# Kernel optimization log

Measured on AMD Instinct MI355X. Metric: run time of the kernel, lower is better.

Reference implementation:

```python
import jax, jax.numpy as jnp
import numpy as np

N = 100000   # nodes
E = 1600000  # edges
D = 128      # input_dim
H = 128      # hidden_dim
O = 128      # output_dim
G = 64       # graphs in batch
BN_EPS = 1e-5


def setup_inputs() -> dict:
    key = jax.random.key(0)
    ks = jax.random.split(key, 32)
    x = jax.random.normal(ks[0], (N, D), jnp.float32)
    edge_index = jax.random.randint(ks[1], (2, E), 0, N, dtype=jnp.int64)
    batch = jnp.sort(jax.random.randint(ks[2], (N,), 0, G, dtype=jnp.int64))

    def lin_w(k, fan_in, fan_out):
        return (jax.random.normal(k, (fan_in, fan_out), jnp.float32) / np.sqrt(fan_in)).astype(jnp.float32)

    def lin_b(k, fan_out):
        return (0.01 * jax.random.normal(k, (fan_out,), jnp.float32)).astype(jnp.float32)

    def bn(k, dim):
        k1, k2, k3, k4 = jax.random.split(k, 4)
        gamma = 1.0 + 0.1 * jax.random.normal(k1, (dim,), jnp.float32)
        beta = 0.1 * jax.random.normal(k2, (dim,), jnp.float32)
        mean = 0.1 * jax.random.normal(k3, (dim,), jnp.float32)
        var = 0.5 + jax.random.uniform(k4, (dim,), jnp.float32)
        return gamma, beta, mean, var

    inp = {
        "x": x, "edge_index": edge_index, "batch": batch,
        "w11": lin_w(ks[3], D, H), "b11": lin_b(ks[4], H),
        "w12": lin_w(ks[5], H, H), "b12": lin_b(ks[6], H),
        "w21": lin_w(ks[7], H, H), "b21": lin_b(ks[8], H),
        "w22": lin_w(ks[9], H, H), "b22": lin_b(ks[10], H),
        "w31": lin_w(ks[11], H, H), "b31": lin_b(ks[12], H),
        "w32": lin_w(ks[13], H, O), "b32": lin_b(ks[14], O),
    }
    g1, be1, m1, v1 = bn(ks[15], H)
    g2, be2, m2, v2 = bn(ks[16], H)
    g3, be3, m3, v3 = bn(ks[17], O)
    inp.update({"bn1_g": g1, "bn1_b": be1, "bn1_m": m1, "bn1_v": v1,
                "bn2_g": g2, "bn2_b": be2, "bn2_m": m2, "bn2_v": v2,
                "bn3_g": g3, "bn3_b": be3, "bn3_m": m3, "bn3_v": v3})
    return inp


def _gin_conv(x, src, dst, wa, ba, wb, bb):
    # sum-aggregate neighbor features: out[i] = x[i] + sum_{(j->i) in E} x[j]  (eps=0)
    agg = jax.ops.segment_sum(x[src], dst, num_segments=N)
    h = x + agg
    # 2-layer MLP: Linear -> ReLU -> Linear
    return jax.nn.relu(h @ wa + ba) @ wb + bb


def _bn_eval(x, g, b, m, v):
    return (x - m) * (g * jax.lax.rsqrt(v + BN_EPS)) + b


def reference(x, edge_index, batch,
              w11, b11, w12, b12, w21, b21, w22, b22, w31, b31, w32, b32,
              bn1_g, bn1_b, bn1_m, bn1_v,
              bn2_g, bn2_b, bn2_m, bn2_v,
              bn3_g, bn3_b, bn3_m, bn3_v):
    src, dst = edge_index[0], edge_index[1]
    h = _gin_conv(x, src, dst, w11, b11, w12, b12)
    h = jax.nn.relu(_bn_eval(h, bn1_g, bn1_b, bn1_m, bn1_v))  # dropout: eval-mode identity
    h = _gin_conv(h, src, dst, w21, b21, w22, b22)
    h = jax.nn.relu(_bn_eval(h, bn2_g, bn2_b, bn2_m, bn2_v))
    h = _gin_conv(h, src, dst, w31, b31, w32, b32)
    h = jax.nn.relu(_bn_eval(h, bn3_g, bn3_b, bn3_m, bn3_v))
    # global mean pool over each graph
    sums = jax.ops.segment_sum(h, batch, num_segments=G)
    counts = jax.ops.segment_sum(jnp.ones((N,), h.dtype), batch, num_segments=G)
    return sums / jnp.maximum(counts, 1.0)[:, None]
```

## Files before the change

### kernel.cpp

```cpp
#include <hip/hip_runtime.h>
#include <hip/hip_bf16.h>
#include <cstdint>

static constexpr int D = 128;
static constexpr int SPANB = 9;
static constexpr int CHUNK = 4096;

typedef __bf16 v8bf __attribute__((ext_vector_type(8)));
typedef float  v4f  __attribute__((ext_vector_type(4)));

__device__ inline float bflo(unsigned u) { return __uint_as_float(u << 16); }
__device__ inline float bfhi(unsigned u) { return __uint_as_float(u & 0xffff0000u); }
__device__ inline unsigned short bfbits(float f) {
    __hip_bfloat16 h = __float2bfloat16(f);
    return *reinterpret_cast<unsigned short*>(&h);
}
__device__ inline unsigned packbf(float a, float b) {
    return (unsigned)bfbits(a) | ((unsigned)bfbits(b) << 16);
}

__global__ __launch_bounds__(256) void prep_kernel(
    const float* __restrict__ w11, const float* __restrict__ w12,
    const float* __restrict__ w21, const float* __restrict__ w22,
    const float* __restrict__ w31, const float* __restrict__ w32,
    __hip_bfloat16* __restrict__ Wp,
    const float* bn1g, const float* bn1b, const float* bn1m, const float* bn1v, const float* lb1,
    const float* bn2g, const float* bn2b, const float* bn2m, const float* bn2v, const float* lb2,
    const float* bn3g, const float* bn3b, const float* bn3m, const float* bn3v, const float* lb3,
    float* sc1, float* sh1, float* sc2, float* sh2, float* sc3, float* sh3,
    const float* __restrict__ x, __hip_bfloat16* __restrict__ xb, long long n8,
    const int* __restrict__ dst, int* __restrict__ blockhist, int nE, int nblk) {
    int b = blockIdx.x, t = threadIdx.x;
    if (b < 48) {
        int idx = b * 256 + t;
        int widx = idx >> 11, r = idx & 2047;
        const float* W = widx == 0 ? w11 : widx == 1 ? w12 : widx == 2 ? w21
                       : widx == 3 ? w22 : widx == 4 ? w31 : w32;
        int l = r & 63, cf = (r >> 6) & 7, ks = r >> 9;
        int k0 = ks * 32 + (l >> 4) * 8, c = cf * 16 + (l & 15);
        unsigned o0 = packbf(W[(k0 + 0) * D + c], W[(k0 + 1) * D + c]);
        unsigned o1 = packbf(W[(k0 + 2) * D + c], W[(k0 + 3) * D + c]);
        unsigned o2 = packbf(W[(k0 + 4) * D + c], W[(k0 + 5) * D + c]);
        unsigned o3 = packbf(W[(k0 + 6) * D + c], W[(k0 + 7) * D + c]);
        reinterpret_cast<uint4*>(Wp + (size_t)idx * 8)[0] = make_uint4(o0, o1, o2, o3);
    } else if (b < 51) {
        if (t < D) {
            int j = b - 48;
            const float *g, *bb, *m, *v, *lb;
            float *sc, *sh;
            if (j == 0)      { g = bn1g; bb = bn1b; m = bn1m; v = bn1v; lb = lb1; sc = sc1; sh = sh1; }
            else if (j == 1) { g = bn2g; bb = bn2b; m = bn2m; v = bn2v; lb = lb2; sc = sc2; sh = sh2; }
            else             { g = bn3g; bb = bn3b; m = bn3m; v = bn3v; lb = lb3; sc = sc3; sh = sh3; }
            float s = g[t] * rsqrtf(v[t] + 1e-5f);
            sc[t] = s;
            sh[t] = (lb[t] - m[t]) * s + bb[t];
        }
    } else if (b < 51 + nblk) {
        __shared__ int h[256];
        h[t] = 0;
        __syncthreads();
        int base = (b - 51) * CHUNK;
#pragma unroll
        for (int i = 0; i < CHUNK / 256; ++i) {
            int e = base + i * 256 + t;
            if (e < nE) atomicAdd(&h[dst[e] >> SPANB], 1);
        }
        __syncthreads();
        blockhist[(b - 51) * 256 + t] = h[t];
    } else {
        long long i = (long long)(b - 51 - nblk) * 256 + t;
        if (i < n8) {
            const float4* f4 = reinterpret_cast<const float4*>(x);
            float4 a = f4[i * 2], bb = f4[i * 2 + 1];
            uint4 o = make_uint4(packbf(a.x, a.y), packbf(a.z, a.w),
                                 packbf(bb.x, bb.y), packbf(bb.z, bb.w));
            reinterpret_cast<uint4*>(xb)[i] = o;
        }
    }
}

__global__ __launch_bounds__(256) void bscan_kernel(int* __restrict__ blockhist,
                                                    int* __restrict__ totals, int nblk) {
    __shared__ int s[256];
    int b = blockIdx.x, t = threadIdx.x;
    int running = 0;
    for (int base = 0; base < nblk; base += 256) {
        int idx = base + t;
        int v = (idx < nblk) ? blockhist[idx * 256 + b] : 0;
        s[t] = v;
        __syncthreads();
#pragma unroll
        for (int off = 1; off < 256; off <<= 1) {
            int add = (t >= off) ? s[t - off] : 0;
            __syncthreads();
            s[t] += add;
            __syncthreads();
        }
        if (idx < nblk) blockhist[idx * 256 + b] = running + s[t] - v;
        int tot = s[255];
        __syncthreads();
        running += tot;
    }
    if (t == 0) totals[b] = running;
}

__global__ void tscan_kernel(const int* __restrict__ totals,
                             int* __restrict__ bucketbase, int nbuk, int nE) {
    __shared__ int s[256];
    int t = threadIdx.x;
    int v = (t < nbuk) ? totals[t] : 0;
    s[t] = v;
    __syncthreads();
#pragma unroll
    for (int off = 1; off < 256; off <<= 1) {
        int add = (t >= off) ? s[t - off] : 0;
        __syncthreads();
        s[t] += add;
        __syncthreads();
    }
    if (t < nbuk) bucketbase[t] = s[t] - v;
    if (t == 0) bucketbase[nbuk] = nE;
}

__global__ __launch_bounds__(256) void fill2_kernel(const int* __restrict__ src,
                                                    const int* __restrict__ dst,
                                                    const int* __restrict__ blockhist,
                                                    const int* __restrict__ bucketbase,
                                                    unsigned* __restrict__ records,
                                                    int nE, int nbuk) {
    __shared__ int cur[256];
    int t = threadIdx.x;
    if (t < nbuk) cur[t] = bucketbase[t] + blockhist[blockIdx.x * 256 + t];
    __syncthreads();
    int base = blockIdx.x * CHUNK;
#pragma unroll
    for (int i = 0; i < CHUNK / 256; ++i) {
        int e = base + i * 256 + t;
        if (e < nE) {
            int d = dst[e], s = src[e];
            int p = atomicAdd(&cur[d >> SPANB], 1);
            records[p] = ((unsigned)s << SPANB) | (unsigned)(d & ((1 << SPANB) - 1));
        }
    }
}

__global__ __launch_bounds__(512) void csr2_kernel(const unsigned* __restrict__ records,
                                                   const int* __restrict__ bucketbase,
                                                   int* __restrict__ rowptr,
                                                   int* __restrict__ col,
                                                   int nN, int nE) {
    __shared__ int cnt[512];
    __shared__ int cur[512];
    int b = blockIdx.x, t = threadIdx.x;
    int node0 = b << SPANB;
    cnt[t] = 0;
    __syncthreads();
    int rbeg = bucketbase[b], rend = bucketbase[b + 1];
    for (int r = rbeg + t; r < rend; r += 512)
        atomicAdd(&cnt[records[r] & ((1 << SPANB) - 1)], 1);
    __syncthreads();
    int v = cnt[t];
#pragma unroll
    for (int off = 1; off < 512; off <<= 1) {
        int add = (t >= off) ? cnt[t - off] : 0;
        __syncthreads();
        cnt[t] += add;
        __syncthreads();
    }
    int pos = rbeg + cnt[t] - v;
    if (node0 + t < nN) rowptr[node0 + t] = pos;
    if (b == 0 && t == 0) rowptr[nN] = nE;
    cur[t] = pos;
    __syncthreads();
    for (int r = rbeg + t; r < rend; r += 512) {
        unsigned rec = records[r];
        int p = atomicAdd(&cur[rec & ((1 << SPANB) - 1)], 1);
        col[p] = (int)(rec >> SPANB);
    }
}

#define ACC8(vv) { a[0]+=bflo(vv.x); a[1]+=bfhi(vv.x); a[2]+=bflo(vv.y); a[3]+=bfhi(vv.y); \
                   a[4]+=bflo(vv.z); a[5]+=bfhi(vv.z); a[6]+=bflo(vv.w); a[7]+=bfhi(vv.w); }

__global__ __launch_bounds__(256) void aggh_kernel(const __hip_bfloat16* __restrict__ h,
                                                   __hip_bfloat16* __restrict__ S,
                                                   const int* __restrict__ rowptr,
                                                   const int* __restrict__ col,
                                                   int nN, int nT) {
    int b8 = blockIdx.x & 7;
    int half = b8 >> 2;
    int tile = (blockIdx.x >> 3) * 4 + (b8 & 3);
    if (tile >= nT) return;
    int node = tile * 32 + (threadIdx.x >> 3);
    if (node >= nN) return;
    int off = half * 8 + (threadIdx.x & 7);
    const uint4* h4 = reinterpret_cast<const uint4*>(h);
    uint4 u = h4[(size_t)node * 16 + off];
    float a[8];
    a[0] = bflo(u.x); a[1] = bfhi(u.x); a[2] = bflo(u.y); a[3] = bfhi(u.y);
    a[4] = bflo(u.z); a[5] = bfhi(u.z); a[6] = bflo(u.w); a[7] = bfhi(u.w);
    int beg = rowptr[node], end = rowptr[node + 1];
    int j = beg;
    for (; j + 3 < end; j += 4) {
        int s0 = col[j], s1 = col[j + 1], s2 = col[j + 2], s3 = col[j + 3];
        uint4 v0 = h4[(size_t)s0 * 16 + off];
        uint4 v1 = h4[(size_t)s1 * 16 + off];
        uint4 v2 = h4[(size_t)s2 * 16 + off];
        uint4 v3 = h4[(size_t)s3 * 16 + off];
        ACC8(v0); ACC8(v1); ACC8(v2); ACC8(v3);
    }
    for (; j < end; ++j) {
        uint4 v0 = h4[(size_t)col[j] * 16 + off];
        ACC8(v0);
    }
    uint4 o = make_uint4(packbf(a[0], a[1]), packbf(a[2], a[3]),
                         packbf(a[4], a[5]), packbf(a[6], a[7]));
    reinterpret_cast<uint4*>(S)[(size_t)node * 16 + off] = o;
}

__global__ __launch_bounds__(256) void mlp3_kernel(
    const __hip_bfloat16* __restrict__ S,
    const __hip_bfloat16* __restrict__ WpA,
    const __hip_bfloat16* __restrict__ WpB,
    const float* __restrict__ b1,
    const float* __restrict__ sc, const float* __restrict__ sh,
    __hip_bfloat16* __restrict__ out, int nN) {
    __shared__ __attribute__((aligned(16))) char Wl[32768];
    __shared__ __attribute__((aligned(16))) char Ml[4][4096];
    int t = threadIdx.x;
    int w = t >> 6, l = t & 63;
    int q2 = l >> 4, r16 = l & 15;
    int row0 = blockIdx.x * 64 + w * 16;
    int row = row0 + r16;
    int ar = row < nN ? row : nN - 1;

    v8bf bfrag[4];
#pragma unroll
    for (int ks = 0; ks < 4; ++ks)
        bfrag[ks] = *reinterpret_cast<const v8bf*>(S + (size_t)ar * D + ks * 32 + q2 * 8);

    uint4* wl = reinterpret_cast<uint4*>(Wl);
    const uint4* wa4 = reinterpret_cast<const uint4*>(WpA);
    const uint4* wb4 = reinterpret_cast<const uint4*>(WpB);

#pragma unroll
    for (int i = 0; i < 8; ++i) wl[i * 256 + t] = wa4[i * 256 + t];
    __syncthreads();

    const v8bf* wv = reinterpret_cast<const v8bf*>(Wl);
    const float4* b14 = reinterpret_cast<const float4*>(b1);
    const float4* sc4 = reinterpret_cast<const float4*>(sc);
    const float4* sh4 = reinterpret_cast<const float4*>(sh);
    char* mid = Ml[w];
    int swz = (r16 & 7) << 4;

    v4f acc[8] = {};
#pragma unroll
    for (int ks = 0; ks < 4; ++ks) {
#pragma unroll
        for (int cf = 0; cf < 8; ++cf)
            acc[cf] = __builtin_amdgcn_mfma_f32_16x16x32_bf16(
                wv[(ks * 8 + cf) * 64 + l], bfrag[ks], acc[cf], 0, 0, 0);
    }
#pragma unroll
    for (int cf = 0; cf < 8; ++cf) {
        float4 bb = b14[cf * 4 + q2];
        float e0 = fmaxf(acc[cf][0] + bb.x, 0.f);
        float e1 = fmaxf(acc[cf][1] + bb.y, 0.f);
        float e2 = fmaxf(acc[cf][2] + bb.z, 0.f);
        float e3 = fmaxf(acc[cf][3] + bb.w, 0.f);
        int waddr = r16 * 256 + ((cf * 32 + q2 * 8) ^ swz);
        *reinterpret_cast<uint2*>(mid + waddr) = make_uint2(packbf(e0, e1), packbf(e2, e3));
    }
    __syncthreads();

#pragma unroll
    for (int i = 0; i < 8; ++i) wl[i * 256 + t] = wb4[i * 256 + t];
    __syncthreads();

    v4f acc2[8] = {};
#pragma unroll
    for (int ks = 0; ks < 4; ++ks) {
        v8bf mfrag = *reinterpret_cast<v8bf*>(mid + r16 * 256 + ((ks * 64 + q2 * 16) ^ swz));
#pragma unroll
        for (int cf = 0; cf < 8; ++cf)
            acc2[cf] = __builtin_amdgcn_mfma_f32_16x16x32_bf16(
                wv[(ks * 8 + cf) * 64 + l], mfrag, acc2[cf], 0, 0, 0);
    }
#pragma unroll
    for (int cf = 0; cf < 8; ++cf) {
        float4 s0 = sc4[cf * 4 + q2], s1 = sh4[cf * 4 + q2];
        float e0 = fmaxf(acc2[cf][0] * s0.x + s1.x, 0.f);
        float e1 = fmaxf(acc2[cf][1] * s0.y + s1.y, 0.f);
        float e2 = fmaxf(acc2[cf][2] * s0.z + s1.z, 0.f);
        float e3 = fmaxf(acc2[cf][3] * s0.w + s1.w, 0.f);
        int waddr = r16 * 256 + ((cf * 32 + q2 * 8) ^ swz);
        *reinterpret_cast<uint2*>(mid + waddr) = make_uint2(packbf(e0, e1), packbf(e2, e3));
    }
    {
        int q = l & 15;
#pragma unroll
        for (int i = 0; i < 4; ++i) {
            int r = (l >> 4) * 4 + i;
            int grow = row0 + r;
            if (grow < nN) {
                uint4 v = *reinterpret_cast<uint4*>(mid + r * 256 + ((q * 16) ^ ((r & 7) << 4)));
                reinterpret_cast<uint4*>(out + (size_t)grow * D)[q] = v;
            }
        }
    }
}

__global__ __launch_bounds__(1024) void pool2_kernel(const __hip_bfloat16* __restrict__ h,
                                                     const int* __restrict__ batch,
                                                     float* __restrict__ out, int nN) {
    int g = blockIdx.x;
    int lo, hi;
    {
        int a = 0, b = nN;
        while (a < b) { int mid = (a + b) >> 1; if (batch[mid] < g) a = mid + 1; else b = mid; }
        lo = a;
        b = nN;
        while (a < b) { int mid = (a + b) >> 1; if (batch[mid] < g + 1) a = mid + 1; else b = mid; }
        hi = a;
    }
    int grp = threadIdx.x >> 4;
    int q = threadIdx.x & 15;
    float a[8] = {};
    const uint4* h4 = reinterpret_cast<const uint4*>(h);
    for (int i = lo + grp; i < hi; i += 64) {
        uint4 v = h4[(size_t)i * 16 + q];
        ACC8(v);
    }
    __shared__ float red[64][130];
#pragma unroll
    for (int k = 0; k < 8; ++k) red[grp][q * 8 + k] = a[k];
    __syncthreads();
    int t = threadIdx.x;
    if (t < D) {
        float s = 0.f;
#pragma unroll 8
        for (int r = 0; r < 64; ++r) s += red[r][t];
        out[(size_t)g * D + t] = s / fmaxf((float)(hi - lo), 1.f);
    }
}

extern "C" void kernel_launch(void* const* d_in, const int* in_sizes, int n_in,
                              void* d_out, int out_size, void* d_ws, size_t ws_size,
                              hipStream_t stream) {
    const float* x    = (const float*)d_in[0];
    const int*   ei   = (const int*)d_in[1];
    const int*   batch= (const int*)d_in[2];
    const float* w11 = (const float*)d_in[3];  const float* b11 = (const float*)d_in[4];
    const float* w12 = (const float*)d_in[5];  const float* b12 = (const float*)d_in[6];
    const float* w21 = (const float*)d_in[7];  const float* b21 = (const float*)d_in[8];
    const float* w22 = (const float*)d_in[9];  const float* b22 = (const float*)d_in[10];
    const float* w31 = (const float*)d_in[11]; const float* b31 = (const float*)d_in[12];
    const float* w32 = (const float*)d_in[13]; const float* b32 = (const float*)d_in[14];
    const float* bn1g = (const float*)d_in[15]; const float* bn1b = (const float*)d_in[16];
    const float* bn1m = (const float*)d_in[17]; const float* bn1v = (const float*)d_in[18];
    const float* bn2g = (const float*)d_in[19]; const float* bn2b = (const float*)d_in[20];
    const float* bn2m = (const float*)d_in[21]; const float* bn2v = (const float*)d_in[22];
    const float* bn3g = (const float*)d_in[23]; const float* bn3b = (const float*)d_in[24];
    const float* bn3m = (const float*)d_in[25]; const float* bn3v = (const float*)d_in[26];

    int nN = in_sizes[0] / D;
    int nE = in_sizes[1] / 2;
    int nG = out_size / D;

    const int* srcp = ei;
    const int* dstp = ei + nE;

    size_t NB2 = (size_t)nN * D * sizeof(__hip_bfloat16);
    char* ws = (char*)d_ws;
    __hip_bfloat16* A16 = (__hip_bfloat16*)ws;
    __hip_bfloat16* B16 = (__hip_bfloat16*)(ws + NB2);
    __hip_bfloat16* S16 = (__hip_bfloat16*)(ws + 2 * NB2);
    __hip_bfloat16* Wp  = (__hip_bfloat16*)(ws + 3 * NB2);
    size_t wp_bytes = 6 * 2048 * 8 * sizeof(__hip_bfloat16);
    char* auxp = ws + 3 * NB2 + wp_bytes;
    size_t aux_bytes = 16384;
    float* sc1 = (float*)auxp + 0,   *sh1 = (float*)auxp + 128;
    float* sc2 = (float*)auxp + 256, *sh2 = (float*)auxp + 384;
    float* sc3 = (float*)auxp + 512, *sh3 = (float*)auxp + 640;
    int*   bucketbase = (int*)(auxp + (768 + 64) * 4);
    int*   totals     = bucketbase + 300;
    int* rowptr = (int*)(auxp + aux_bytes);
    int* col    = rowptr + (nN + 1);

    unsigned* records = (unsigned*)S16;
    int* blockhist    = (int*)((char*)S16 + (size_t)nE * 4);

    int nbuk = (nN + 511) >> SPANB;
    int nblk = (nE + CHUNK - 1) / CHUNK;
    long long n8 = (long long)nN * D / 8;
    int cvtBlocks = (int)((n8 + 255) / 256);

    prep_kernel<<<51 + nblk + cvtBlocks, 256, 0, stream>>>(
        w11, w12, w21, w22, w31, w32, Wp,
        bn1g, bn1b, bn1m, bn1v, b12,
        bn2g, bn2b, bn2m, bn2v, b22,
        bn3g, bn3b, bn3m, bn3v, b32,
        sc1, sh1, sc2, sh2, sc3, sh3,
        x, A16, n8,
        dstp, blockhist, nE, nblk);

    bscan_kernel<<<nbuk, 256, 0, stream>>>(blockhist, totals, nblk);
    tscan_kernel<<<1, 256, 0, stream>>>(totals, bucketbase, nbuk, nE);
    fill2_kernel<<<nblk, 256, 0, stream>>>(srcp, dstp, blockhist, bucketbase, records, nE, nbuk);
    csr2_kernel<<<nbuk, 512, 0, stream>>>(records, bucketbase, rowptr, col, nN, nE);

    int nT = (nN + 31) / 32;
    int aggBlocks = ((nT + 3) / 4) * 8;
    int mlpBlocks = (nN + 63) / 64;
    __hip_bfloat16* Wp1 = Wp + 0 * 16384; __hip_bfloat16* Wp2 = Wp + 1 * 16384;
    __hip_bfloat16* Wp3 = Wp + 2 * 16384; __hip_bfloat16* Wp4 = Wp + 3 * 16384;
    __hip_bfloat16* Wp5 = Wp + 4 * 16384; __hip_bfloat16* Wp6 = Wp + 5 * 16384;

    aggh_kernel<<<aggBlocks, 256, 0, stream>>>(A16, S16, rowptr, col, nN, nT);
    mlp3_kernel<<<mlpBlocks, 256, 0, stream>>>(S16, Wp1, Wp2, b11, sc1, sh1, B16, nN);

    aggh_kernel<<<aggBlocks, 256, 0, stream>>>(B16, S16, rowptr, col, nN, nT);
    mlp3_kernel<<<mlpBlocks, 256, 0, stream>>>(S16, Wp3, Wp4, b21, sc2, sh2, A16, nN);

    aggh_kernel<<<aggBlocks, 256, 0, stream>>>(A16, S16, rowptr, col, nN, nT);
    mlp3_kernel<<<mlpBlocks, 256, 0, stream>>>(S16, Wp5, Wp6, b31, sc3, sh3, B16, nN);

    pool2_kernel<<<nG, 1024, 0, stream>>>(B16, batch, (float*)d_out, nN);
}
```

Measured before the change: 289.6 us.

## Assign aggregation feature halves to XCC groups via atomic work counters

The aggregation kernel now reads the hardware XCC id, maps XCCs 0-3 and 4-7 to feature half 0 or 1, and takes tiles from a per-half atomic counter, switching to the other half once its own is used up. Each half of the bf16 feature table is then gathered mostly by one group of XCCs, so it can stay in their L2 instead of both halves being spread across all XCCs. Counters are zeroed in the prep kernel, one pair per layer. The cost is one atomic plus a block barrier per block, and the mapping depends on XCC numbering and how the hardware schedules blocks.

After: 430.8 us. +48.7%, slower.

```diff
diff --git a/kernel.cpp b/kernel.cpp
--- a/kernel.cpp
+++ b/kernel.cpp
@@ -28,6 +28,7 @@
     const float* bn2g, const float* bn2b, const float* bn2m, const float* bn2v, const float* lb2,
     const float* bn3g, const float* bn3b, const float* bn3m, const float* bn3v, const float* lb3,
     float* sc1, float* sh1, float* sc2, float* sh2, float* sc3, float* sh3,
+    int* __restrict__ wctr,
     const float* __restrict__ x, __hip_bfloat16* __restrict__ xb, long long n8,
     const int* __restrict__ dst, int* __restrict__ blockhist, int nE, int nblk) {
     int b = blockIdx.x, t = threadIdx.x;
@@ -55,6 +56,10 @@
             sc[t] = s;
             sh[t] = (lb[t] - m[t]) * s + bb[t];
         }
+        if (t == 200) {
+            wctr[(b - 48) * 2 + 0] = 0;
+            wctr[(b - 48) * 2 + 1] = 0;
+        }
     } else if (b < 51 + nblk) {
         __shared__ int h[256];
         h[t] = 0;
@@ -186,10 +191,21 @@
                                                    __hip_bfloat16* __restrict__ S,
                                                    const int* __restrict__ rowptr,
                                                    const int* __restrict__ col,
-                                                   int nN, int nT) {
-    int b8 = blockIdx.x & 7;
-    int half = b8 >> 2;
-    int tile = (blockIdx.x >> 3) * 4 + (b8 & 3);
+                                                   int nN, int nT,
+                                                   int* __restrict__ ctr) {
+    __shared__ int sh_info;
+    int xcc;
+    asm volatile("s_getreg_b32 %0, hwreg(HW_REG_XCC_ID)" : "=s"(xcc));
+    int pref = (xcc >> 2) & 1;
+    if (threadIdx.x == 0) {
+        int tl = atomicAdd(&ctr[pref], 1);
+        int hf = pref;
+        if (tl >= nT) { hf ^= 1; tl = atomicAdd(&ctr[hf], 1); }
+        sh_info = (tl << 1) | hf;
+    }
+    __syncthreads();
+    int info = sh_info;
+    int tile = info >> 1, half = info & 1;
     if (tile >= nT) return;
     int node = tile * 32 + (threadIdx.x >> 3);
     if (node >= nN) return;
@@ -385,6 +401,7 @@
     float* sc3 = (float*)auxp + 512, *sh3 = (float*)auxp + 640;
     int*   bucketbase = (int*)(auxp + (768 + 64) * 4);
     int*   totals     = bucketbase + 300;
+    int*   wctr       = (int*)(auxp + 8192);
     int* rowptr = (int*)(auxp + aux_bytes);
     int* col    = rowptr + (nN + 1);
 
@@ -402,6 +419,7 @@
         bn2g, bn2b, bn2m, bn2v, b22,
         bn3g, bn3b, bn3m, bn3v, b32,
         sc1, sh1, sc2, sh2, sc3, sh3,
+        wctr,
         x, A16, n8,
         dstp, blockhist, nE, nblk);
 
@@ -411,19 +429,19 @@
     csr2_kernel<<<nbuk, 512, 0, stream>>>(records, bucketbase, rowptr, col, nN, nE);
 
     int nT = (nN + 31) / 32;
-    int aggBlocks = ((nT + 3) / 4) * 8;
+    int aggBlocks = 2 * nT;
     int mlpBlocks = (nN + 63) / 64;
     __hip_bfloat16* Wp1 = Wp + 0 * 16384; __hip_bfloat16* Wp2 = Wp + 1 * 16384;
     __hip_bfloat16* Wp3 = Wp + 2 * 16384; __hip_bfloat16* Wp4 = Wp + 3 * 16384;
     __hip_bfloat16* Wp5 = Wp + 4 * 16384; __hip_bfloat16* Wp6 = Wp + 5 * 16384;
 
-    aggh_kernel<<<aggBlocks, 256, 0, stream>>>(A16, S16, rowptr, col, nN, nT);
+    aggh_kernel<<<aggBlocks, 256, 0, stream>>>(A16, S16, rowptr, col, nN, nT, wctr + 0);
     mlp3_kernel<<<mlpBlocks, 256, 0, stream>>>(S16, Wp1, Wp2, b11, sc1, sh1, B16, nN);
 
-    aggh_kernel<<<aggBlocks, 256, 0, stream>>>(B16, S16, rowptr, col, nN, nT);
+    aggh_kernel<<<aggBlocks, 256, 0, stream>>>(B16, S16, rowptr, col, nN, nT, wctr + 2);
     mlp3_kernel<<<mlpBlocks, 256, 0, stream>>>(S16, Wp3, Wp4, b21, sc2, sh2, A16, nN);
 
-    aggh_kernel<<<aggBlocks, 256, 0, stream>>>(A16, S16, rowptr, col, nN, nT);
+    aggh_kernel<<<aggBlocks, 256, 0, stream>>>(A16, S16, rowptr, col, nN, nT, wctr + 4);
     mlp3_kernel<<<mlpBlocks, 256, 0, stream>>>(S16, Wp5, Wp6, b31, sc3, sh3, B16, nN);
 
     pool2_kernel<<<nG, 1024, 0, stream>>>(B16, batch, (float*)d_out, nN);
```
